# Optimization experiments

Hardware: AMD Instinct MI355X
Metric: run time of the kernel (lower is better)

Reference implementation:

```python
import jax, jax.numpy as jnp
import numpy as np

B, N, F, H, E = 8, 10000, 256, 128, 320000
P_DROP = 0.5

def setup_inputs() -> dict:
    key = jax.random.key(0)
    kx, ku, kr, kc, kv, kw = jax.random.split(key, 6)
    x = jax.random.normal(kx, (B, N, F), dtype=jnp.float32)
    drop_u = jax.random.uniform(ku, (B, N, F), dtype=jnp.float32)
    rows = jax.random.randint(kr, (B, E), 0, N, dtype=jnp.int64)
    cols = jax.random.randint(kc, (B, E), 0, N, dtype=jnp.int64)
    vals = jax.random.uniform(kv, (B, E), dtype=jnp.float32)
    weight = jax.random.normal(kw, (F, H), dtype=jnp.float32)
    return {"x": x, "drop_u": drop_u, "rows": rows, "cols": cols, "vals": vals, "weight": weight}

def _spmm(rows, cols, vals, dense):
    # out[r] += vals * dense[c]  -> A @ dense for one graph
    gathered = vals[:, None] * dense[cols]          # [E, H]
    return jax.ops.segment_sum(gathered, rows, num_segments=N)  # [N, H]

def reference(x, drop_u, rows, cols, vals, weight):
    # inverted dropout, p=0.5
    mask = (drop_u > P_DROP).astype(x.dtype)
    xd = x * mask * (1.0 / (1.0 - P_DROP))          # [B, N, F]
    xw = jnp.einsum('bnf,fh->bnh', xd, weight)      # [B, N, H]
    out = jax.vmap(_spmm)(rows, cols, vals, xw)     # [B, N, H]
    return out
```

## Files before the change

kernel.cpp:

```cpp
#include <hip/hip_runtime.h>
#include <hip/hip_bf16.h>

#define DEVINL __device__ __forceinline__

constexpr int Bb = 8;
constexpr int Nn = 10000;
constexpr int Ff = 256;
constexpr int Hh = 128;
constexpr int Ee = 320000;
constexpr int Mm = Bb * Nn;

constexpr int CHUNK = 64;
constexpr int NCH = (Nn + CHUNK - 1) / CHUNK;
constexpr int CAP = 2560;
constexpr int GPB = 80;
constexpr int EPG = Ee / GPB;
constexpr int TW_BLOCKS = (Ff * Hh) / 256;

typedef __attribute__((ext_vector_type(8))) short short8;
typedef __attribute__((ext_vector_type(4))) float float4v;
typedef __attribute__((ext_vector_type(4))) unsigned short ushort4v;

DEVINL unsigned short f2b(float f) {
    unsigned int u;
    __builtin_memcpy(&u, &f, 4);
    unsigned int r = (u + 0x7fffu + ((u >> 16) & 1u)) >> 16;
    return (unsigned short)r;
}
DEVINL float i2f(int i) {
    float f;
    __builtin_memcpy(&f, &i, 4);
    return f;
}
DEVINL float lo_bf(unsigned int two) {
    unsigned int u = two << 16;
    float f;
    __builtin_memcpy(&f, &u, 4);
    return f;
}
DEVINL float hi_bf(unsigned int two) {
    unsigned int u = two & 0xffff0000u;
    float f;
    __builtin_memcpy(&f, &u, 4);
    return f;
}

__global__ __launch_bounds__(256) void bucket2_kernel(const int* __restrict__ rows,
                                                      const int* __restrict__ cols,
                                                      const float* __restrict__ vals,
                                                      int* __restrict__ cur,
                                                      int2* __restrict__ bkt,
                                                      const float* __restrict__ w,
                                                      unsigned short* __restrict__ wT) {
    int t = threadIdx.x;
    if (blockIdx.x >= Bb * GPB) {
        int idx = (blockIdx.x - Bb * GPB) * 256 + t;
        if (idx < Ff * Hh) {
            int h = idx / Ff, k = idx % Ff;
            wT[idx] = f2b(w[(size_t)k * Hh + h]);
        }
        return;
    }
    __shared__ int2 sedge[EPG];
    __shared__ int lcnt[NCH];
    __shared__ int lofs[NCH];
    __shared__ int lcur[NCH];
    __shared__ int gall[NCH];
    __shared__ int wsum[4];
    int raw = blockIdx.x;
    int b = raw & 7;
    int g = raw >> 3;
    const int base = b * Ee + g * EPG;

    for (int j = t; j < NCH; j += 256) lcnt[j] = 0;
    __syncthreads();
    for (int i = t; i < EPG; i += 256)
        atomicAdd(&lcnt[rows[base + i] >> 6], 1);
    __syncthreads();
    {
        int lane = t & 63, wv = t >> 6;
        int v = (t < NCH) ? lcnt[t] : 0;
        int incl = v;
#pragma unroll
        for (int d = 1; d < 64; d <<= 1) {
            int o = __shfl_up(incl, d);
            if (lane >= d) incl += o;
        }
        if (lane == 63) wsum[wv] = incl;
        __syncthreads();
        if (t == 0) {
            int s = 0;
#pragma unroll
            for (int k = 0; k < 4; k++) { int x = wsum[k]; wsum[k] = s; s += x; }
        }
        __syncthreads();
        if (t < NCH) {
            int ex = incl - v + wsum[wv];
            lofs[t] = ex;
            lcur[t] = ex;
        }
    }
    __syncthreads();
    for (int j = t; j < NCH; j += 256) {
        int gb = atomicAdd(&cur[b * NCH + j], lcnt[j]);
        gall[j] = gb - lofs[j];
    }
    __syncthreads();
    for (int i = t; i < EPG; i += 256) {
        int r = rows[base + i];
        int c = cols[base + i];
        float vf = vals[base + i];
        int vb;
        __builtin_memcpy(&vb, &vf, 4);
        int bk = r >> 6;
        int p = atomicAdd(&lcur[bk], 1);
        sedge[p] = make_int2(((r & 63) << 26) | (c << 8) | bk, vb);
    }
    __syncthreads();
    for (int i = t; i < EPG; i += 256) {
        int2 e = sedge[i];
        int j = e.x & 0xff;
        int slot = gall[j] + i;
        if (slot < CAP)
            bkt[(size_t)(b * NCH + j) * CAP + slot] = e;
    }
}

__global__ __launch_bounds__(256, 3) void gemm_kernel(const float* __restrict__ x,
                                                      const float* __restrict__ u,
                                                      const unsigned short* __restrict__ wT,
                                                      unsigned short* __restrict__ xw) {
    __shared__ unsigned short sA[64 * 136];
    __shared__ unsigned short sB[128 * 136];
    int t = threadIdx.x;
    int wave = t >> 6, lane = t & 63;
    int n = lane & 15, q = lane >> 4;
    int m0 = blockIdx.x * 64;

    float4v acc[8];
#pragma unroll
    for (int i = 0; i < 8; i++) acc[i] = {0.f, 0.f, 0.f, 0.f};

    for (int kh = 0; kh < 2; kh++) {
#pragma unroll
        for (int i = 0; i < 8; i++) {
            int idx = t + i * 256;
            int row = idx >> 5;
            int c4 = idx & 31;
            const float* xp = x + (size_t)(m0 + row) * Ff + kh * 128 + c4 * 4;
            const float* up = u + (size_t)(m0 + row) * Ff + kh * 128 + c4 * 4;
            float4 xv = *(const float4*)xp;
            float4 uv = *(const float4*)up;
            ushort4v a;
            a.x = f2b(uv.x > 0.5f ? xv.x * 2.0f : 0.0f);
            a.y = f2b(uv.y > 0.5f ? xv.y * 2.0f : 0.0f);
            a.z = f2b(uv.z > 0.5f ? xv.z * 2.0f : 0.0f);
            a.w = f2b(uv.w > 0.5f ? xv.w * 2.0f : 0.0f);
            *(ushort4v*)(&sA[row * 136 + c4 * 4]) = a;
        }
#pragma unroll
        for (int i = 0; i < 8; i++) {
            int idx = t + i * 256;
            int h = idx >> 4;
            int kc = idx & 15;
            short8 bv = *(const short8*)(wT + (size_t)h * Ff + kh * 128 + kc * 8);
            *(short8*)(&sB[h * 136 + kc * 8]) = bv;
        }
        __syncthreads();
#pragma unroll
        for (int k0 = 0; k0 < 128; k0 += 32) {
            short8 af = *(const short8*)(&sA[(wave * 16 + n) * 136 + k0 + q * 8]);
#pragma unroll
            for (int tt = 0; tt < 8; tt++) {
                short8 bf = *(const short8*)(&sB[(tt * 16 + n) * 136 + k0 + q * 8]);
                acc[tt] = __builtin_amdgcn_mfma_f32_16x16x32_bf16(af, bf, acc[tt], 0, 0, 0);
            }
        }
        __syncthreads();
    }
#pragma unroll
    for (int tt = 0; tt < 8; tt++) {
#pragma unroll
        for (int r = 0; r < 4; r++) {
            int row = m0 + wave * 16 + q * 4 + r;
            int col = tt * 16 + n;
            xw[(size_t)row * Hh + col] = f2b(acc[tt][r]);
        }
    }
}

__global__ __launch_bounds__(256) void spmm_kernel(const int* __restrict__ cur,
                                                   const int2* __restrict__ bkt,
                                                   const unsigned short* __restrict__ xw,
                                                   float* __restrict__ out) {
    __shared__ int2 ssort[CAP];
    __shared__ int rh[CHUNK];
    __shared__ int roff[CHUNK];
    __shared__ int rcur[CHUNK];
    int raw = blockIdx.x;
    int blk = (raw & 7) * NCH + (raw >> 3);
    int b = blk / NCH, ch = blk % NCH;
    int t = threadIdx.x, w = t >> 6, lane = t & 63;

    if (t < CHUNK) rh[t] = 0;
    __syncthreads();
    int cnt = cur[blk];
    if (cnt > CAP) cnt = CAP;
    const int2* pe = bkt + (size_t)blk * CAP;

    for (int i = t; i < cnt; i += 256)
        atomicAdd(&rh[((unsigned)pe[i].x) >> 26], 1);
    __syncthreads();
    if (w == 0) {
        int v = rh[lane];
        int s = v;
#pragma unroll
        for (int d = 1; d < 64; d <<= 1) {
            int o = __shfl_up(s, d);
            if (lane >= d) s += o;
        }
        roff[lane] = s - v;
        rcur[lane] = s - v;
    }
    __syncthreads();
    for (int i = t; i < cnt; i += 256) {
        int2 e = pe[i];
        int p = atomicAdd(&rcur[((unsigned)e.x) >> 26], 1);
        ssort[p] = make_int2(e.x & 0x3FFF00, e.y);
    }
    __syncthreads();

    const char* xwb = (const char*)(xw + (size_t)b * Nn * Hh);
    int lane4 = lane * 4;
    for (int rr = 0; rr < 16; rr++) {
        int rl = w * 16 + rr;
        int r = ch * CHUNK + rl;
        if (r >= Nn) break;
        int off = roff[rl];
        int rcnt = rh[rl];

        float a0[4], a1[4];
#pragma unroll
        for (int k = 0; k < 4; k++) { a0[k] = 0.f; a1[k] = 0.f; }

        int mn = rcnt & ~3;
        for (int i = 0; i < mn; i += 4) {
#pragma unroll
            for (int k = 0; k < 4; k++) {
                int2 e = ssort[off + i + k];
                unsigned int two = *(const unsigned int*)(xwb + (unsigned)(e.x + lane4));
                float v = i2f(e.y);
                a0[k] += v * lo_bf(two);
                a1[k] += v * hi_bf(two);
            }
        }
        for (int i = mn; i < rcnt; i++) {
            int2 e = ssort[off + i];
            unsigned int two = *(const unsigned int*)(xwb + (unsigned)(e.x + lane4));
            float v = i2f(e.y);
            a0[i - mn] += v * lo_bf(two);
            a1[i - mn] += v * hi_bf(two);
        }
        float s0 = (a0[0] + a0[1]) + (a0[2] + a0[3]);
        float s1 = (a1[0] + a1[1]) + (a1[2] + a1[3]);
        float2 res;
        res.x = s0;
        res.y = s1;
        *(float2*)(out + ((size_t)b * Nn + r) * Hh + lane * 2) = res;
    }
}

extern "C" void kernel_launch(void* const* d_in, const int* in_sizes, int n_in,
                              void* d_out, int out_size, void* d_ws, size_t ws_size,
                              hipStream_t stream) {
    const float* x    = (const float*)d_in[0];
    const float* du   = (const float*)d_in[1];
    const int*   rows = (const int*)d_in[2];
    const int*   cols = (const int*)d_in[3];
    const float* vals = (const float*)d_in[4];
    const float* w    = (const float*)d_in[5];
    float*       out  = (float*)d_out;

    char* p = (char*)d_ws;
    unsigned short* xw = (unsigned short*)p; p += (size_t)Mm * Hh * 2;
    unsigned short* wT = (unsigned short*)p; p += (size_t)Ff * Hh * 2;
    int* cur   = (int*)p; p += (size_t)Bb * NCH * 4;
    int2* bkt  = (int2*)p; p += (size_t)Bb * NCH * CAP * 8;

    hipMemsetAsync(cur, 0, (size_t)Bb * NCH * 4, stream);
    bucket2_kernel<<<Bb * GPB + TW_BLOCKS, 256, 0, stream>>>(rows, cols, vals, cur, bkt, w, wT);
    gemm_kernel<<<Mm / 64, 256, 0, stream>>>(x, du, wT, xw);
    spmm_kernel<<<Bb * NCH, 256, 0, stream>>>(cur, bkt, xw, out);
}
```

Before: 288.9 us.

## Pre-swizzle weights into MFMA fragment order and read B directly from global

The weight transpose now writes bf16 weights in the exact per-lane MFMA B-fragment order. The GEMM kernel reads each B fragment straight from global memory (L2/L1 cached, 64KB total) instead of staging a 128x136 tile in shared memory. This removes the sB staging loads and cuts LDS use, so the launch bound is raised from 3 to 6 blocks per CU. In exchange every MFMA operand now comes from a global load whose latency has to be hidden by the higher occupancy.

```diff
diff --git a/kernel.cpp b/kernel.cpp
--- a/kernel.cpp
+++ b/kernel.cpp
@@ -51,13 +51,18 @@
                                                       int* __restrict__ cur,
                                                       int2* __restrict__ bkt,
                                                       const float* __restrict__ w,
-                                                      unsigned short* __restrict__ wT) {
+                                                      unsigned short* __restrict__ wF) {
     int t = threadIdx.x;
     if (blockIdx.x >= Bb * GPB) {
         int idx = (blockIdx.x - Bb * GPB) * 256 + t;
         if (idx < Ff * Hh) {
-            int h = idx / Ff, k = idx % Ff;
-            wT[idx] = f2b(w[(size_t)k * Hh + h]);
+            int j = idx & 7;
+            int lane = (idx >> 3) & 63;
+            int tt = (idx >> 9) & 7;
+            int ksl = idx >> 12;
+            int k = ksl * 32 + (lane >> 4) * 8 + j;
+            int h = tt * 16 + (lane & 15);
+            wF[idx] = f2b(w[(size_t)k * Hh + h]);
         }
         return;
     }
@@ -126,12 +131,11 @@
     }
 }
 
-__global__ __launch_bounds__(256, 3) void gemm_kernel(const float* __restrict__ x,
+__global__ __launch_bounds__(256, 6) void gemm_kernel(const float* __restrict__ x,
                                                       const float* __restrict__ u,
-                                                      const unsigned short* __restrict__ wT,
+                                                      const unsigned short* __restrict__ wF,
                                                       unsigned short* __restrict__ xw) {
     __shared__ unsigned short sA[64 * 136];
-    __shared__ unsigned short sB[128 * 136];
     int t = threadIdx.x;
     int wave = t >> 6, lane = t & 63;
     int n = lane & 15, q = lane >> 4;
@@ -158,21 +162,14 @@
             a.w = f2b(uv.w > 0.5f ? xv.w * 2.0f : 0.0f);
             *(ushort4v*)(&sA[row * 136 + c4 * 4]) = a;
         }
-#pragma unroll
-        for (int i = 0; i < 8; i++) {
-            int idx = t + i * 256;
-            int h = idx >> 4;
-            int kc = idx & 15;
-            short8 bv = *(const short8*)(wT + (size_t)h * Ff + kh * 128 + kc * 8);
-            *(short8*)(&sB[h * 136 + kc * 8]) = bv;
-        }
         __syncthreads();
 #pragma unroll
         for (int k0 = 0; k0 < 128; k0 += 32) {
             short8 af = *(const short8*)(&sA[(wave * 16 + n) * 136 + k0 + q * 8]);
+            const unsigned short* wfb = wF + (size_t)(kh * 4 + (k0 >> 5)) * 4096 + lane * 8;
 #pragma unroll
             for (int tt = 0; tt < 8; tt++) {
-                short8 bf = *(const short8*)(&sB[(tt * 16 + n) * 136 + k0 + q * 8]);
+                short8 bf = *(const short8*)(wfb + tt * 512);
                 acc[tt] = __builtin_amdgcn_mfma_f32_16x16x32_bf16(af, bf, acc[tt], 0, 0, 0);
             }
         }
@@ -182,9 +179,9 @@
     for (int tt = 0; tt < 8; tt++) {
 #pragma unroll
         for (int r = 0; r < 4; r++) {
-            int row = m0 + wave * 16 + q * 4 + r;
+            int orow = m0 + wave * 16 + q * 4 + r;
             int col = tt * 16 + n;
-            xw[(size_t)row * Hh + col] = f2b(acc[tt][r]);
+            xw[(size_t)orow * Hh + col] = f2b(acc[tt][r]);
         }
     }
 }
@@ -283,12 +280,12 @@
 
     char* p = (char*)d_ws;
     unsigned short* xw = (unsigned short*)p; p += (size_t)Mm * Hh * 2;
-    unsigned short* wT = (unsigned short*)p; p += (size_t)Ff * Hh * 2;
+    unsigned short* wF = (unsigned short*)p; p += (size_t)Ff * Hh * 2;
     int* cur   = (int*)p; p += (size_t)Bb * NCH * 4;
     int2* bkt  = (int2*)p; p += (size_t)Bb * NCH * CAP * 8;
 
     hipMemsetAsync(cur, 0, (size_t)Bb * NCH * 4, stream);
-    bucket2_kernel<<<Bb * GPB + TW_BLOCKS, 256, 0, stream>>>(rows, cols, vals, cur, bkt, w, wT);
-    gemm_kernel<<<Mm / 64, 256, 0, stream>>>(x, du, wT, xw);
+    bucket2_kernel<<<Bb * GPB + TW_BLOCKS, 256, 0, stream>>>(rows, cols, vals, cur, bkt, w, wF);
+    gemm_kernel<<<Mm / 64, 256, 0, stream>>>(x, du, wF, xw);
     spmm_kernel<<<Bb * NCH, 256, 0, stream>>>(cur, bkt, xw, out);
 }
```

New measurement: 295.4 us. 2.3% more time.
